# Performance work log

Hardware: AMD Instinct MI355X
Metric: run time of the kernel (lower is better)

The kernel has to match this reference:

```python
import jax, jax.numpy as jnp
import numpy as np

S = 8192      # total packed tokens
H = 1152      # hidden size
NH = 16       # heads
HD = 72       # head dim
NSEG = 8      # number of packed (equal-length) sequences
L = S // NSEG # tokens per sequence
SCALE = HD ** -0.5


def setup_inputs() -> dict:
    key = jax.random.key(0)
    ks = jax.random.split(key, 4)
    hidden_states = jax.random.normal(ks[0], (1, S, H), jnp.float32)
    # Real rotary cos/sin per token position within each sequence.
    inv_freq = 1.0 / (10000.0 ** (np.arange(0, HD, 2, dtype=np.float64) / HD))
    freqs = np.outer(np.arange(L, dtype=np.float64), inv_freq)  # [L, HD/2]
    emb = np.concatenate([freqs, freqs], axis=-1)               # [L, HD]
    cos = jnp.asarray(np.tile(np.cos(emb), (NSEG, 1)), jnp.float32)  # [S, HD]
    sin = jnp.asarray(np.tile(np.sin(emb), (NSEG, 1)), jnp.float32)
    Wqkv = jax.random.normal(ks[1], (H, 3 * H), jnp.float32) * (H ** -0.5)
    bqkv = jnp.zeros((3 * H,), jnp.float32)
    Wout = jax.random.normal(ks[2], (H, H), jnp.float32) * (H ** -0.5)
    bout = jnp.zeros((H,), jnp.float32)
    cu_seqlens = jnp.arange(NSEG + 1, dtype=jnp.int32) * L
    return dict(hidden_states=hidden_states, cos=cos, sin=sin,
                Wqkv=Wqkv, bqkv=bqkv, Wout=Wout, bout=bout,
                cu_seqlens=cu_seqlens)


def _rotate_half(x):
    return jnp.concatenate([-x[..., HD // 2:], x[..., :HD // 2]], axis=-1)


def reference(hidden_states, cos, sin, Wqkv, bqkv, Wout, bout, cu_seqlens):
    # QKV projection (fused)
    qkv = hidden_states @ Wqkv + bqkv                 # [1, S, 3H]
    q, k, v = jnp.split(qkv, [H, 2 * H], axis=-1)
    q = q.reshape(1, S, NH, HD)
    k = k.reshape(1, S, NH, HD)
    v = v.reshape(1, S, NH, HD)
    # Inline RoPE on q/k (cos/sin broadcast over heads)
    c = cos[None, :, None, :]
    s = sin[None, :, None, :]
    q = q * c + _rotate_half(q) * s
    k = k * c + _rotate_half(k) * s
    # Varlen (block-diagonal) non-causal attention: equal-length segments
    q = q.reshape(NSEG, L, NH, HD)
    k = k.reshape(NSEG, L, NH, HD)
    v = v.reshape(NSEG, L, NH, HD)
    scores = jnp.einsum('nqhd,nkhd->nhqk', q, k) * SCALE  # [NSEG, NH, L, L]
    probs = jax.nn.softmax(scores, axis=-1)
    ctx = jnp.einsum('nhqk,nkhd->nqhd', probs, v)         # [NSEG, L, NH, HD]
    ctx = ctx.reshape(1, S, H)
    # Output projection
    return ctx @ Wout + bout
```

## Files before the change

kernel.cpp:

```cpp
#include <hip/hip_runtime.h>
#include <hip/hip_fp16.h>
#include <cstdint>

typedef _Float16 half8 __attribute__((ext_vector_type(8)));
typedef _Float16 half4 __attribute__((ext_vector_type(4)));
typedef float floatx4 __attribute__((ext_vector_type(4)));

#define S_TOT 8192
#define H_DIM 1152
#define NHEAD 16
#define HD 72
#define QSTR 96
#define KSTR 104
#define PSTR 76
#define VSTR 76
#define VT_TILE 6080
#define NSEG 8
#define SEGL 1024
#define QSCALE 0.17002324631230988f

__device__ __forceinline__ void gld_lds16(const void* g, void* l) {
  __builtin_amdgcn_global_load_lds((const __attribute__((address_space(1))) void*)g,
                                   (__attribute__((address_space(3))) void*)l, 16, 0, 0);
}

__global__ void cast_f32_f16(const float* __restrict__ in, _Float16* __restrict__ out, int n) {
  int i = (blockIdx.x * 256 + threadIdx.x) * 4;
  if (i < n) {
    float4 v = *(const float4*)(in + i);
    half4 o = { (_Float16)v.x, (_Float16)v.y, (_Float16)v.z, (_Float16)v.w };
    *(half4*)(out + i) = o;
  }
}

__global__ void transpose_cast(const float* __restrict__ W, _Float16* __restrict__ Wt,
                               int R, int C) {
  __shared__ float tile[32][33];
  int tx = threadIdx.x, ty = threadIdx.y;
  int bx = blockIdx.x, by = blockIdx.y;
#pragma unroll
  for (int i = 0; i < 4; ++i)
    tile[ty + i * 8][tx] = W[(size_t)(by * 32 + ty + i * 8) * C + bx * 32 + tx];
  __syncthreads();
#pragma unroll
  for (int i = 0; i < 4; ++i)
    Wt[(size_t)(bx * 32 + ty + i * 8) * R + by * 32 + tx] = (_Float16)tile[tx][ty + i * 8];
}

template <bool OUT_HALF>
__global__ __launch_bounds__(256) void gemm_bt(
    const _Float16* __restrict__ A, const _Float16* __restrict__ Bt,
    const float* __restrict__ bias, float* __restrict__ Cf, _Float16* __restrict__ Ch,
    int M, int N, int K, int NT) {
  __shared__ __align__(16) _Float16 As[128 * 72];
  __shared__ __align__(16) _Float16 Bs[128 * 72];
  const int tid = threadIdx.x;
  const int lane = tid & 63, w = tid >> 6;
  const int quad = lane >> 4, l16 = lane & 15;
  const int wm = w >> 1, wn = w & 1;
  const int id = blockIdx.x;
  const int j = id & 7, k = id >> 3;
  const int nt_ = k % NT, mt_ = (k / NT) * 8 + j;
  const int m0 = mt_ * 128, n0 = nt_ * 128;

  int rowi[5], cci[5];
#pragma unroll
  for (int i = 0; i < 5; ++i) {
    int c = tid + i * 256;
    int r = c / 9, cc = c - r * 9;
    rowi[i] = r;
    cci[i] = (cc == 8) ? 0 : cc;
  }

  floatx4 acc[4][4] = {};

  for (int kt = 0; kt < K; kt += 64) {
    __syncthreads();
#pragma unroll
    for (int i = 0; i < 4; ++i) {
      gld_lds16(A + (size_t)(m0 + rowi[i]) * K + kt + cci[i] * 8, (char*)As + (tid + i * 256) * 16);
      gld_lds16(Bt + (size_t)(n0 + rowi[i]) * K + kt + cci[i] * 8, (char*)Bs + (tid + i * 256) * 16);
    }
    if (tid < 128) {
      gld_lds16(A + (size_t)(m0 + rowi[4]) * K + kt + cci[4] * 8, (char*)As + (tid + 1024) * 16);
      gld_lds16(Bt + (size_t)(n0 + rowi[4]) * K + kt + cci[4] * 8, (char*)Bs + (tid + 1024) * 16);
    }
    __syncthreads();
#pragma unroll
    for (int kk = 0; kk < 2; ++kk) {
      half8 af[4], bf[4];
#pragma unroll
      for (int im = 0; im < 4; ++im)
        af[im] = *(const half8*)&As[(wm * 64 + im * 16 + l16) * 72 + kk * 32 + quad * 8];
#pragma unroll
      for (int in = 0; in < 4; ++in)
        bf[in] = *(const half8*)&Bs[(wn * 64 + in * 16 + l16) * 72 + kk * 32 + quad * 8];
#pragma unroll
      for (int im = 0; im < 4; ++im)
#pragma unroll
        for (int in = 0; in < 4; ++in)
          acc[im][in] = __builtin_amdgcn_mfma_f32_16x16x32_f16(af[im], bf[in], acc[im][in], 0, 0, 0);
    }
  }
#pragma unroll
  for (int im = 0; im < 4; ++im) {
    int m = m0 + wm * 64 + im * 16 + quad * 4;
#pragma unroll
    for (int in = 0; in < 4; ++in) {
      int n = n0 + wn * 64 + in * 16 + l16;
      float b = bias[n];
#pragma unroll
      for (int r = 0; r < 4; ++r) {
        float v = acc[im][in][r] + b;
        if (OUT_HALF) Ch[(size_t)(m + r) * N + n] = (_Float16)v;
        else          Cf[(size_t)(m + r) * N + n] = v;
      }
    }
  }
}

__global__ void rope_scatter(const _Float16* __restrict__ QKV,
                             const float* __restrict__ cosb,
                             const float* __restrict__ sinb,
                             _Float16* __restrict__ Qo, _Float16* __restrict__ Ko) {
  int t = blockIdx.x * 256 + threadIdx.x;
  int l = t & 1023, h = (t >> 10) & 15, n = t >> 14;
  int s = n * SEGL + l;
  const _Float16* q = QKV + (size_t)s * 3456 + h * HD;
  const _Float16* k = q + H_DIM;
  const float* cs = cosb + (size_t)s * HD;
  const float* sn = sinb + (size_t)s * HD;
  size_t qo = (size_t)t * QSTR, ko = (size_t)t * KSTR;
  half8 z = {};
  {
    _Float16 qr[72], qv[72];
#pragma unroll
    for (int i = 0; i < 9; ++i) *(half8*)&qr[8 * i] = *(const half8*)(q + 8 * i);
#pragma unroll
    for (int d = 0; d < 36; ++d) {
      float c0 = cs[d], s0 = sn[d], c1 = cs[d + 36], s1 = sn[d + 36];
      float a = (float)qr[d], b = (float)qr[d + 36];
      qv[d]      = (_Float16)((a * c0 - b * s0) * QSCALE);
      qv[d + 36] = (_Float16)((b * c1 + a * s1) * QSCALE);
    }
#pragma unroll
    for (int i = 0; i < 9; ++i) *(half8*)(Qo + qo + 8 * i) = *(half8*)&qv[8 * i];
#pragma unroll
    for (int i = 9; i < 12; ++i) *(half8*)(Qo + qo + 8 * i) = z;
  }
  {
    _Float16 kr[72], kv[72];
#pragma unroll
    for (int i = 0; i < 9; ++i) *(half8*)&kr[8 * i] = *(const half8*)(k + 8 * i);
#pragma unroll
    for (int d = 0; d < 36; ++d) {
      float c0 = cs[d], s0 = sn[d], c1 = cs[d + 36], s1 = sn[d + 36];
      float a = (float)kr[d], b = (float)kr[d + 36];
      kv[d]      = (_Float16)(a * c0 - b * s0);
      kv[d + 36] = (_Float16)(b * c1 + a * s1);
    }
#pragma unroll
    for (int i = 0; i < 9; ++i) *(half8*)(Ko + ko + 8 * i) = *(half8*)&kv[8 * i];
#pragma unroll
    for (int i = 9; i < 13; ++i) *(half8*)(Ko + ko + 8 * i) = z;
  }
}

__global__ __launch_bounds__(256) void transpose_v(const _Float16* __restrict__ QKV,
                                                   _Float16* __restrict__ Vt) {
  __shared__ __align__(16) _Float16 Vs[64 * 88];
  const int tid = threadIdx.x;
  const int kb = blockIdx.x, h = blockIdx.y, n = blockIdx.z;
  const int s0 = n * SEGL + kb * 64;
  const _Float16* src = QKV + (size_t)s0 * 3456 + 2 * H_DIM + h * HD;
  for (int idx = tid; idx < 576; idx += 256) {
    int key = idx / 9, c = idx - key * 9;
    *(half8*)&Vs[key * 88 + c * 8] = *(const half8*)(src + (size_t)key * 3456 + c * 8);
  }
  __syncthreads();
  _Float16* dst = Vt + (((size_t)(n * NHEAD + h)) * 16 + kb) * VT_TILE;
  for (int idx = tid; idx < 800; idx += 256) {
    int d = idx / 10, c = idx - d * 10;
    if (c < 9) {
      half8 v = {};
      if (d < HD) {
#pragma unroll
        for (int j = 0; j < 8; ++j) v[j] = Vs[(c * 8 + j) * 88 + d];
      }
      *(half8*)(dst + d * VSTR + c * 8) = v;
    } else {
      *(half4*)(dst + d * VSTR + 72) = half4{};
    }
  }
}

__global__ __launch_bounds__(256) void attn_kernel(
    const _Float16* __restrict__ Qb, const _Float16* __restrict__ Kb,
    const _Float16* __restrict__ Vtb, _Float16* __restrict__ Ctx) {
  __shared__ __align__(16) _Float16 Kt[64 * KSTR];
  __shared__ __align__(16) _Float16 Vt[80 * VSTR];
  __shared__ __align__(16) _Float16 Ps[4 * 64 * PSTR];
  const int tid = threadIdx.x;
  const int lane = tid & 63, w = tid >> 6;
  const int quad = lane >> 4, l16 = lane & 15;
  const int id = blockIdx.x;
  const int hn = id & 127, qb = id >> 7;
  const int h = hn >> 3, n = hn & 7;
  const size_t hseg = (size_t)(n * NHEAD + h);
  const _Float16* Qg = Qb + hseg * SEGL * QSTR;
  const _Float16* Kg = Kb + hseg * SEGL * KSTR;
  const _Float16* Vg = Vtb + hseg * 16 * VT_TILE;

  half8 qf[4][3];
#pragma unroll
  for (int qg = 0; qg < 4; ++qg) {
    int row = qb * 256 + w * 64 + qg * 16 + l16;
#pragma unroll
    for (int kc = 0; kc < 3; ++kc)
      qf[qg][kc] = *(const half8*)(Qg + (size_t)row * QSTR + kc * 32 + quad * 8);
  }
  float l_s[4] = {0.f, 0.f, 0.f, 0.f};
  floatx4 o_acc[4][5] = {};

  for (int kb = 0; kb < SEGL / 64; ++kb) {
    __syncthreads();
    {
      const char* base = (const char*)(Kg + (size_t)kb * 64 * KSTR);
#pragma unroll
      for (int i = 0; i < 3; ++i)
        gld_lds16(base + tid * 16 + i * 4096, (char*)Kt + tid * 16 + i * 4096);
      if (tid < 64)
        gld_lds16(base + 12288 + tid * 16, (char*)Kt + 12288 + tid * 16);
    }
    {
      const char* base = (const char*)(Vg + (size_t)kb * VT_TILE);
#pragma unroll
      for (int i = 0; i < 2; ++i)
        gld_lds16(base + tid * 16 + i * 4096, (char*)Vt + tid * 16 + i * 4096);
      if (tid < 248)
        gld_lds16(base + 8192 + tid * 16, (char*)Vt + 8192 + tid * 16);
    }
    __syncthreads();
    floatx4 sa[4][4] = {};
#pragma unroll
    for (int nt = 0; nt < 4; ++nt) {
      half8 kf[3];
#pragma unroll
      for (int kc = 0; kc < 3; ++kc)
        kf[kc] = *(const half8*)&Kt[(nt * 16 + l16) * KSTR + kc * 32 + quad * 8];
#pragma unroll
      for (int qg = 0; qg < 4; ++qg)
#pragma unroll
        for (int kc = 0; kc < 3; ++kc)
          sa[qg][nt] = __builtin_amdgcn_mfma_f32_16x16x32_f16(kf[kc], qf[qg][kc], sa[qg][nt], 0, 0, 0);
    }
#pragma unroll
    for (int qg = 0; qg < 4; ++qg) {
      float sum = 0.f;
#pragma unroll
      for (int nt = 0; nt < 4; ++nt)
#pragma unroll
        for (int r = 0; r < 4; ++r) {
          float p = exp2f(sa[qg][nt][r]);
          sa[qg][nt][r] = p;
          sum += p;
        }
      sum += __shfl_xor(sum, 16, 64);
      sum += __shfl_xor(sum, 32, 64);
      l_s[qg] += sum;
      int prow = (w * 64 + qg * 16 + l16) * PSTR;
#pragma unroll
      for (int nt = 0; nt < 4; ++nt) {
        half4 ph = { (_Float16)sa[qg][nt][0], (_Float16)sa[qg][nt][1],
                     (_Float16)sa[qg][nt][2], (_Float16)sa[qg][nt][3] };
        *(half4*)&Ps[prow + nt * 16 + quad * 4] = ph;
      }
    }
#pragma unroll
    for (int kc2 = 0; kc2 < 2; ++kc2) {
      half8 vf[5];
#pragma unroll
      for (int t = 0; t < 5; ++t)
        vf[t] = *(const half8*)&Vt[(t * 16 + l16) * VSTR + kc2 * 32 + quad * 8];
#pragma unroll
      for (int qg = 0; qg < 4; ++qg) {
        half8 pb = *(const half8*)&Ps[(w * 64 + qg * 16 + l16) * PSTR + kc2 * 32 + quad * 8];
#pragma unroll
        for (int t = 0; t < 5; ++t)
          o_acc[qg][t] = __builtin_amdgcn_mfma_f32_16x16x32_f16(vf[t], pb, o_acc[qg][t], 0, 0, 0);
      }
    }
  }
#pragma unroll
  for (int qg = 0; qg < 4; ++qg) {
    float rl = 1.0f / l_s[qg];
    size_t s2 = (size_t)n * SEGL + qb * 256 + w * 64 + qg * 16 + l16;
#pragma unroll
    for (int t = 0; t < 5; ++t) {
      int d0 = t * 16 + quad * 4;
      if (d0 < HD) {
        half4 hv = { (_Float16)(o_acc[qg][t][0] * rl), (_Float16)(o_acc[qg][t][1] * rl),
                     (_Float16)(o_acc[qg][t][2] * rl), (_Float16)(o_acc[qg][t][3] * rl) };
        *(half4*)&Ctx[s2 * H_DIM + h * HD + d0] = hv;
      }
    }
  }
}

extern "C" void kernel_launch(void* const* d_in, const int* in_sizes, int n_in,
                              void* d_out, int out_size, void* d_ws, size_t ws_size,
                              hipStream_t stream) {
  const float* X    = (const float*)d_in[0];
  const float* cosb = (const float*)d_in[1];
  const float* sinb = (const float*)d_in[2];
  const float* Wqkv = (const float*)d_in[3];
  const float* bqkv = (const float*)d_in[4];
  const float* Wout = (const float*)d_in[5];
  const float* bout = (const float*)d_in[6];
  float* out = (float*)d_out;
  char* ws = (char*)d_ws;

  _Float16* Xb   = (_Float16*)(ws);
  _Float16* Wqt  = (_Float16*)(ws + 18874368);
  _Float16* Wot  = (_Float16*)(ws + 26836992);
  _Float16* QKVb = (_Float16*)(ws + 29491200);
  _Float16* Qb   = (_Float16*)(ws + 86114304);
  _Float16* Kb   = (_Float16*)(ws + 111280128);
  _Float16* Vtb  = (_Float16*)(ws + 138543104);
  _Float16* Ctx  = Xb;

  cast_f32_f16<<<9216, 256, 0, stream>>>(X, Xb, S_TOT * H_DIM);
  transpose_cast<<<dim3(108, 36), dim3(32, 8), 0, stream>>>(Wqkv, Wqt, H_DIM, 3 * H_DIM);
  transpose_cast<<<dim3(36, 36), dim3(32, 8), 0, stream>>>(Wout, Wot, H_DIM, H_DIM);
  gemm_bt<true><<<1728, 256, 0, stream>>>(Xb, Wqt, bqkv, nullptr, QKVb,
                                          S_TOT, 3 * H_DIM, H_DIM, 27);
  rope_scatter<<<512, 256, 0, stream>>>(QKVb, cosb, sinb, Qb, Kb);
  transpose_v<<<dim3(16, 16, 8), 256, 0, stream>>>(QKVb, Vtb);
  attn_kernel<<<512, 256, 0, stream>>>(Qb, Kb, Vtb, Ctx);
  gemm_bt<false><<<576, 256, 0, stream>>>(Ctx, Wot, bout, out, nullptr,
                                          S_TOT, H_DIM, H_DIM, 9);
}
```

Before: 422.5 us.

## Compute softmax row sums via ones column in V and halve per-block query tile

The V-transpose kernel now writes a row of ones at padded dimension 72, so the P·V MFMA accumulates the softmax denominator in the fifth output tile. This removes the explicit exp-sum reduction and cross-lane shuffles. The attention block now covers 128 queries instead of 256, with 2 query groups per wave, a smaller P scratch buffer and twice as many blocks, and it asks for 3 blocks per CU. The tradeoff is that each block reloads the K/V tiles for half as many queries, and the denominator is summed from fp16-rounded P values.

```diff
diff --git a/kernel.cpp b/kernel.cpp
--- a/kernel.cpp
+++ b/kernel.cpp
@@ -181,25 +181,30 @@
   _Float16* dst = Vt + (((size_t)(n * NHEAD + h)) * 16 + kb) * VT_TILE;
   for (int idx = tid; idx < 800; idx += 256) {
     int d = idx / 10, c = idx - d * 10;
-    if (c < 9) {
+    if (c < 8) {
       half8 v = {};
       if (d < HD) {
 #pragma unroll
         for (int j = 0; j < 8; ++j) v[j] = Vs[(c * 8 + j) * 88 + d];
+      } else if (d == HD) {
+#pragma unroll
+        for (int j = 0; j < 8; ++j) v[j] = (_Float16)1.0f;
       }
       *(half8*)(dst + d * VSTR + c * 8) = v;
+    } else if (c == 8) {
+      *(half8*)(dst + d * VSTR + 64) = half8{};
     } else {
       *(half4*)(dst + d * VSTR + 72) = half4{};
     }
   }
 }
 
-__global__ __launch_bounds__(256) void attn_kernel(
+__global__ __launch_bounds__(256, 3) void attn_kernel(
     const _Float16* __restrict__ Qb, const _Float16* __restrict__ Kb,
     const _Float16* __restrict__ Vtb, _Float16* __restrict__ Ctx) {
   __shared__ __align__(16) _Float16 Kt[64 * KSTR];
   __shared__ __align__(16) _Float16 Vt[80 * VSTR];
-  __shared__ __align__(16) _Float16 Ps[4 * 64 * PSTR];
+  __shared__ __align__(16) _Float16 Ps[4 * 16 * PSTR];
   const int tid = threadIdx.x;
   const int lane = tid & 63, w = tid >> 6;
   const int quad = lane >> 4, l16 = lane & 15;
@@ -211,16 +216,15 @@
   const _Float16* Kg = Kb + hseg * SEGL * KSTR;
   const _Float16* Vg = Vtb + hseg * 16 * VT_TILE;
 
-  half8 qf[4][3];
-#pragma unroll
-  for (int qg = 0; qg < 4; ++qg) {
-    int row = qb * 256 + w * 64 + qg * 16 + l16;
+  half8 qf[2][3];
+#pragma unroll
+  for (int qg = 0; qg < 2; ++qg) {
+    int row = qb * 128 + w * 32 + qg * 16 + l16;
 #pragma unroll
     for (int kc = 0; kc < 3; ++kc)
       qf[qg][kc] = *(const half8*)(Qg + (size_t)row * QSTR + kc * 32 + quad * 8);
   }
-  float l_s[4] = {0.f, 0.f, 0.f, 0.f};
-  floatx4 o_acc[4][5] = {};
+  floatx4 o_acc[2][5] = {};
 
   for (int kb = 0; kb < SEGL / 64; ++kb) {
     __syncthreads();
@@ -241,7 +245,7 @@
         gld_lds16(base + 8192 + tid * 16, (char*)Vt + 8192 + tid * 16);
     }
     __syncthreads();
-    floatx4 sa[4][4] = {};
+    floatx4 sa[2][4] = {};
 #pragma unroll
     for (int nt = 0; nt < 4; ++nt) {
       half8 kf[3];
@@ -249,52 +253,47 @@
       for (int kc = 0; kc < 3; ++kc)
         kf[kc] = *(const half8*)&Kt[(nt * 16 + l16) * KSTR + kc * 32 + quad * 8];
 #pragma unroll
-      for (int qg = 0; qg < 4; ++qg)
+      for (int qg = 0; qg < 2; ++qg)
 #pragma unroll
         for (int kc = 0; kc < 3; ++kc)
           sa[qg][nt] = __builtin_amdgcn_mfma_f32_16x16x32_f16(kf[kc], qf[qg][kc], sa[qg][nt], 0, 0, 0);
     }
 #pragma unroll
-    for (int qg = 0; qg < 4; ++qg) {
-      float sum = 0.f;
+    for (int qg = 0; qg < 2; ++qg)
 #pragma unroll
       for (int nt = 0; nt < 4; ++nt)
 #pragma unroll
-        for (int r = 0; r < 4; ++r) {
-          float p = exp2f(sa[qg][nt][r]);
-          sa[qg][nt][r] = p;
-          sum += p;
-        }
-      sum += __shfl_xor(sum, 16, 64);
-      sum += __shfl_xor(sum, 32, 64);
-      l_s[qg] += sum;
-      int prow = (w * 64 + qg * 16 + l16) * PSTR;
+        for (int r = 0; r < 4; ++r)
+          sa[qg][nt][r] = exp2f(sa[qg][nt][r]);
+    half8 vf[2][5];
+#pragma unroll
+    for (int kc2 = 0; kc2 < 2; ++kc2)
+#pragma unroll
+      for (int t = 0; t < 5; ++t)
+        vf[kc2][t] = *(const half8*)&Vt[(t * 16 + l16) * VSTR + kc2 * 32 + quad * 8];
+#pragma unroll
+    for (int qg = 0; qg < 2; ++qg) {
+      int prow = (w * 16 + l16) * PSTR;
 #pragma unroll
       for (int nt = 0; nt < 4; ++nt) {
         half4 ph = { (_Float16)sa[qg][nt][0], (_Float16)sa[qg][nt][1],
                      (_Float16)sa[qg][nt][2], (_Float16)sa[qg][nt][3] };
         *(half4*)&Ps[prow + nt * 16 + quad * 4] = ph;
       }
-    }
-#pragma unroll
-    for (int kc2 = 0; kc2 < 2; ++kc2) {
-      half8 vf[5];
-#pragma unroll
-      for (int t = 0; t < 5; ++t)
-        vf[t] = *(const half8*)&Vt[(t * 16 + l16) * VSTR + kc2 * 32 + quad * 8];
-#pragma unroll
-      for (int qg = 0; qg < 4; ++qg) {
-        half8 pb = *(const half8*)&Ps[(w * 64 + qg * 16 + l16) * PSTR + kc2 * 32 + quad * 8];
+#pragma unroll
+      for (int kc2 = 0; kc2 < 2; ++kc2) {
+        half8 pb = *(const half8*)&Ps[(w * 16 + l16) * PSTR + kc2 * 32 + quad * 8];
 #pragma unroll
         for (int t = 0; t < 5; ++t)
-          o_acc[qg][t] = __builtin_amdgcn_mfma_f32_16x16x32_f16(vf[t], pb, o_acc[qg][t], 0, 0, 0);
-      }
-    }
-  }
-#pragma unroll
-  for (int qg = 0; qg < 4; ++qg) {
-    float rl = 1.0f / l_s[qg];
-    size_t s2 = (size_t)n * SEGL + qb * 256 + w * 64 + qg * 16 + l16;
+          o_acc[qg][t] = __builtin_amdgcn_mfma_f32_16x16x32_f16(vf[kc2][t], pb, o_acc[qg][t], 0, 0, 0);
+      }
+    }
+  }
+#pragma unroll
+  for (int qg = 0; qg < 2; ++qg) {
+    float lsum = __shfl(o_acc[qg][4][0], 32 + l16, 64);
+    float rl = 1.0f / lsum;
+    size_t s2 = (size_t)n * SEGL + qb * 128 + w * 32 + qg * 16 + l16;
 #pragma unroll
     for (int t = 0; t < 5; ++t) {
       int d0 = t * 16 + quad * 4;
@@ -336,7 +335,7 @@
                                           S_TOT, 3 * H_DIM, H_DIM, 27);
   rope_scatter<<<512, 256, 0, stream>>>(QKVb, cosb, sinb, Qb, Kb);
   transpose_v<<<dim3(16, 16, 8), 256, 0, stream>>>(QKVb, Vtb);
-  attn_kernel<<<512, 256, 0, stream>>>(Qb, Kb, Vtb, Ctx);
+  attn_kernel<<<1024, 256, 0, stream>>>(Qb, Kb, Vtb, Ctx);
   gemm_bt<false><<<576, 256, 0, stream>>>(Ctx, Wot, bout, out, nullptr,
                                           S_TOT, H_DIM, H_DIM, 9);
 }
```

After: 400.1 us. -5.3%, faster.
